# Kernel optimization log

Measured on AMD Instinct MI355X. Metric: run time of the kernel, lower is better.

The kernel has to match this reference:

```python
import jax, jax.numpy as jnp
import numpy as np

B, N, FEAT, MSG, LINK_H, CLS = 8, 128, 1024, 256, 512, 600
PROP = 2  # propagate_layers


def setup_inputs() -> dict:
    key = jax.random.key(0)
    ks = jax.random.split(key, 16)
    g = lambda k, shape, s=0.02: jax.random.normal(k, shape, dtype=jnp.float32) * s
    inp = {
        'edge_features': g(ks[0], (B, N, N, FEAT), 1.0),
        'node_features': g(ks[1], (B, N, FEAT), 1.0),
        'adj_mat': jnp.zeros((B, N, N), jnp.float32),          # shape placeholder only
        'node_labels': jnp.zeros((B, N, CLS), jnp.float32),    # shape placeholder only
        'human_nums': 64,
        'obj_nums': 64,
        # feature resize linears (Linear(FEAT -> MSG))
        'W_er': g(ks[2], (MSG, FEAT)), 'b_er': jnp.zeros((MSG,), jnp.float32),
        'W_nr': g(ks[3], (MSG, FEAT)), 'b_nr': jnp.zeros((MSG,), jnp.float32),
        # link fun (GraphConv): 1x1 Conv2d(MSG->LINK_H), ReLU, 1x1 Conv2d(LINK_H->1)
        'W_l1': g(ks[4], (LINK_H, MSG)), 'b_l1': jnp.zeros((LINK_H,), jnp.float32),
        'W_l2': g(ks[5], (1, LINK_H)), 'b_l2': jnp.zeros((1,), jnp.float32),
        # message fun linear_concat_relu: Linear(node+edge = 2*MSG -> MSG), ReLU
        'W_m': g(ks[6], (MSG, 2 * MSG)), 'b_m': jnp.zeros((MSG,), jnp.float32),
        # GRU(input=MSG, hidden=MSG), single layer single step
        'W_ih': g(ks[7], (3 * MSG, MSG)), 'b_ih': jnp.zeros((3 * MSG,), jnp.float32),
        'W_hh': g(ks[8], (3 * MSG, MSG)), 'b_hh': jnp.zeros((3 * MSG,), jnp.float32),
        # readout fc: Linear(MSG -> CLS)
        'W_r': g(ks[9], (CLS, MSG)), 'b_r': jnp.zeros((CLS,), jnp.float32),
    }
    return inp


def reference(edge_features, node_features, adj_mat, node_labels,
              human_nums, obj_nums,
              W_er, b_er, W_nr, b_nr, W_l1, b_l1, W_l2, b_l2,
              W_m, b_m, W_ih, b_ih, W_hh, b_hh, W_r, b_r):
    # valid_node_num = human_nums + obj_nums == N for every batch element.
    # Resize raw features to message size.
    e = edge_features @ W_er.T + b_er        # [B, v, w, MSG]
    h = node_features @ W_nr.T + b_nr        # [B, w, MSG]  (node states are never rewritten in source)
    # Split concat-linear into two matmuls to avoid materializing [B,N,N,2*MSG].
    W_mh, W_me = W_m[:, :MSG], W_m[:, MSG:]
    msg_h = jnp.einsum('bwd,md->bwm', h, W_mh)                 # node part, shared over target v
    msg_e = jnp.einsum('bvwd,md->bvwm', e, W_me) + b_m          # edge part (original e, constant over rounds)
    edge_state = e
    m = None
    pred_adj = None
    for _ in range(PROP):
        # link fun: per-(v,w) MLP over channels (1x1 convs)
        x = jax.nn.relu(edge_state @ W_l1.T + b_l1)             # [B,v,w,LINK_H]
        pred_adj = (x @ W_l2.T + b_l2)[..., 0]                  # [B,N,N]
        sig = jax.nn.sigmoid(pred_adj)
        # message fun linear_concat_relu, gated by predicted adjacency
        m = jax.nn.relu(msg_h[:, None, :, :] + msg_e)           # [B,v,w,MSG]
        m = sig[..., None] * m
        # hidden_edge_states[round+1][:, :, w, v] = m_v[:, :, w]
        edge_state = jnp.swapaxes(m, 1, 2)
    # node update happens per node each round but hidden node states are never
    # written back in the source, so only the last round's GRU step matters.
    m_sum = m.sum(axis=2)                                       # [B,v,MSG]
    gi = m_sum @ W_ih.T + b_ih
    gh = h @ W_hh.T + b_hh
    ir, iz, inn = jnp.split(gi, 3, axis=-1)
    hr, hz, hn = jnp.split(gh, 3, axis=-1)
    r = jax.nn.sigmoid(ir + hr)
    z = jax.nn.sigmoid(iz + hz)
    n = jnp.tanh(inn + r * hn)
    h_new = (1.0 - z) * n + z * h                               # [B,N,MSG]
    pred_node_labels = h_new @ W_r.T + b_r                      # [B,N,CLS]
    return pred_adj, pred_node_labels
```

## Files before the change

kernel.cpp:

```cpp
#include <hip/hip_runtime.h>
#include <cstdint>
#include <cstddef>

#define NND   128
#define FEATD 1024
#define MSGD  256
#define LHD   512
#define CLSD  600
#define LDST  264

typedef __bf16 bf16_t;
typedef bf16_t bf16x8 __attribute__((ext_vector_type(8)));
typedef float  f32x4  __attribute__((ext_vector_type(4)));
typedef unsigned short u16;
typedef u16 u16x8 __attribute__((ext_vector_type(8)));
typedef u16 u16x4 __attribute__((ext_vector_type(4)));

static __device__ __forceinline__ float bf2f(u16 u) {
  union { unsigned u; float f; } x; x.u = ((unsigned)u) << 16; return x.f;
}
static __device__ __forceinline__ u16 f2bf(float f) {
  union { float f; unsigned u; } x; x.f = f;
  return (u16)((x.u + 0x7fffu + ((x.u >> 16) & 1u)) >> 16);
}
static __device__ __forceinline__ f32x4 mfma16(u16x8 a, u16x8 b, f32x4 c) {
  return __builtin_amdgcn_mfma_f32_16x16x32_bf16(
      __builtin_bit_cast(bf16x8, a), __builtin_bit_cast(bf16x8, b), c, 0, 0, 0);
}
static __device__ __forceinline__ f32x4 zero4() {
  f32x4 v; v[0] = 0.f; v[1] = 0.f; v[2] = 0.f; v[3] = 0.f; return v;
}
static __device__ __forceinline__ float sigm(float x) { return 1.0f / (1.0f + expf(-x)); }

__global__ void k_cvt(const float* __restrict__ src, u16* __restrict__ dst, int n) {
  int i = (blockIdx.x * 256 + threadIdx.x) * 4;
  if (i + 3 < n) {
    float4 f = *(const float4*)(src + i);
    u16x4 o; o[0] = f2bf(f.x); o[1] = f2bf(f.y); o[2] = f2bf(f.z); o[3] = f2bf(f.w);
    *(u16x4*)(dst + i) = o;
  }
}

__global__ __launch_bounds__(256) void k_comb(const float* __restrict__ Wm,
                                              const float* __restrict__ Wer,
                                              const float* __restrict__ b_er,
                                              const float* __restrict__ b_m,
                                              u16* __restrict__ WcombB,
                                              float* __restrict__ bcomb) {
  const int m = blockIdx.x >> 2, ch = blockIdx.x & 3;
  const int d = ch * 256 + threadIdx.x;
  float s = 0.f;
  for (int k = 0; k < 256; ++k)
    s += Wm[(size_t)m * 512 + 256 + k] * Wer[(size_t)k * FEATD + d];
  WcombB[(size_t)m * FEATD + d] = f2bf(s);
  if (ch == 0 && threadIdx.x == 0) {
    float bb2 = b_m[m];
    for (int k = 0; k < 256; ++k) bb2 += Wm[(size_t)m * 512 + 256 + k] * b_er[k];
    bcomb[m] = bb2;
  }
}

__global__ __launch_bounds__(256) void s1_hmsg(const float* __restrict__ node,
                                               const float* __restrict__ Wnr,
                                               const float* __restrict__ bnr,
                                               const float* __restrict__ Wm,
                                               float* __restrict__ h32,
                                               u16* __restrict__ msghB) {
  __shared__ float nrow[FEATD];
  __shared__ float hrow[MSGD];
  const int r = blockIdx.x;
  const int t = threadIdx.x;
  *(float4*)(&nrow[t * 4]) = *(const float4*)(node + (size_t)r * FEATD + t * 4);
  __syncthreads();
  float acc = bnr[t];
  for (int d = 0; d < FEATD; ++d) acc += nrow[d] * Wnr[(size_t)t * FEATD + d];
  h32[(size_t)r * MSGD + t] = acc;
  hrow[t] = acc;
  __syncthreads();
  float mh = 0.f;
  for (int k = 0; k < MSGD; ++k) mh += hrow[k] * Wm[(size_t)t * 2 * MSGD + k];
  msghB[(size_t)r * MSGD + t] = f2bf(mh);
}

__global__ __launch_bounds__(256, 2) void k_main(
    const float* __restrict__ edge, const u16* __restrict__ Wer, const u16* __restrict__ Wm,
    const u16* __restrict__ Wl1, const float* __restrict__ b_er, const float* __restrict__ b_m,
    const float* __restrict__ b_l1, const float* __restrict__ W_l2, const float* __restrict__ b_l2,
    const u16* __restrict__ msgh, u16* __restrict__ M0g, float* __restrict__ pa_out) {
  __shared__ __align__(16) u16 lsE[64][LDST];
  __shared__ __align__(16) u16 lsM[64][LDST];
  __shared__ float lsPA[4][64];
  __shared__ float lsSig[64];

  const int tid = threadIdx.x, lane = tid & 63, wave = tid >> 6;
  const int lh = lane & 15, lq = lane >> 4;
  const int base = blockIdx.x * 64;
  const int bb = base >> 14, vv = (base >> 7) & 127, w0 = base & 127;

  f32x4 acc[4][4];
#pragma unroll
  for (int m = 0; m < 4; ++m)
#pragma unroll
    for (int t = 0; t < 4; ++t) acc[m][t] = zero4();

  const int srow = tid >> 2;
  const int scq  = (tid & 3) * 16;
  const float* esrc = edge + (size_t)(base + srow) * FEATD + scq;
  float4 lda[4], ldb[4];

  auto LOADS_A = [&](int s) {
#pragma unroll
    for (int i = 0; i < 4; ++i) lda[i] = *(const float4*)(esrc + s * 64 + i * 4);
  };
  auto LOADS_B = [&](int s) {
#pragma unroll
    for (int i = 0; i < 4; ++i) ldb[i] = *(const float4*)(esrc + s * 64 + i * 4);
  };
  auto WRITES = [&](const float4* ld, int slot) {
    u16* wp = &lsE[srow][slot * 64 + scq];
    u16x8 o0, o1;
    o0[0] = f2bf(ld[0].x); o0[1] = f2bf(ld[0].y); o0[2] = f2bf(ld[0].z); o0[3] = f2bf(ld[0].w);
    o0[4] = f2bf(ld[1].x); o0[5] = f2bf(ld[1].y); o0[6] = f2bf(ld[1].z); o0[7] = f2bf(ld[1].w);
    o1[0] = f2bf(ld[2].x); o1[1] = f2bf(ld[2].y); o1[2] = f2bf(ld[2].z); o1[3] = f2bf(ld[2].w);
    o1[4] = f2bf(ld[3].x); o1[5] = f2bf(ld[3].y); o1[6] = f2bf(ld[3].z); o1[7] = f2bf(ld[3].w);
    *(u16x8*)wp = o0;
    *(u16x8*)(wp + 8) = o1;
  };
  auto MSTEP = [&](int sk, int slot) {
#pragma unroll
    for (int ks = 0; ks < 2; ++ks) {
      u16x8 afr[4];
#pragma unroll
      for (int m = 0; m < 4; ++m)
        afr[m] = *(const u16x8*)(&lsE[16 * m + lh][slot * 64 + ks * 32 + lq * 8]);
      const int kg = sk * 64 + ks * 32 + lq * 8;
#pragma unroll
      for (int t = 0; t < 4; ++t) {
        int col = wave * 64 + t * 16 + lh;
        u16x8 bfr = *(const u16x8*)(Wer + (size_t)col * FEATD + kg);
#pragma unroll
        for (int m = 0; m < 4; ++m) acc[m][t] = mfma16(afr[m], bfr, acc[m][t]);
      }
    }
  };

  LOADS_A(0);
  LOADS_B(1);
  for (int s2 = 0; s2 < 16; s2 += 2) {
    WRITES(lda, 0);
    if (s2 + 2 < 16) LOADS_A(s2 + 2);
    __syncthreads();
    MSTEP(s2, 0);
    WRITES(ldb, 1);
    if (s2 + 3 < 16) LOADS_B(s2 + 3);
    __syncthreads();
    MSTEP(s2 + 1, 1);
  }
  __syncthreads();
#pragma unroll
  for (int t = 0; t < 4; ++t) {
    int col = wave * 64 + t * 16 + lh;
    float be = b_er[col];
#pragma unroll
    for (int m = 0; m < 4; ++m)
#pragma unroll
      for (int j = 0; j < 4; ++j)
        lsE[16 * m + 4 * lq + j][col] = f2bf(acc[m][t][j] + be);
  }
  __syncthreads();

  float prow[4][4];
#pragma unroll
  for (int m = 0; m < 4; ++m)
#pragma unroll
    for (int j = 0; j < 4; ++j) prow[m][j] = 0.f;
#pragma unroll
  for (int np = 0; np < 2; ++np) {
#pragma unroll
    for (int m = 0; m < 4; ++m)
#pragma unroll
      for (int t = 0; t < 4; ++t) acc[m][t] = zero4();
#pragma unroll
    for (int ks = 0; ks < 8; ++ks) {
      u16x8 afr[4];
#pragma unroll
      for (int m = 0; m < 4; ++m) afr[m] = *(const u16x8*)(&lsE[16 * m + lh][ks * 32 + lq * 8]);
      const int kg = ks * 32 + lq * 8;
#pragma unroll
      for (int t = 0; t < 4; ++t) {
        int col = wave * 128 + np * 64 + t * 16 + lh;
        u16x8 bfr = *(const u16x8*)(Wl1 + (size_t)col * MSGD + kg);
#pragma unroll
        for (int m = 0; m < 4; ++m) acc[m][t] = mfma16(afr[m], bfr, acc[m][t]);
      }
    }
#pragma unroll
    for (int t = 0; t < 4; ++t) {
      int col = wave * 128 + np * 64 + t * 16 + lh;
      float bl = b_l1[col], wl = W_l2[col];
#pragma unroll
      for (int m = 0; m < 4; ++m)
#pragma unroll
        for (int j = 0; j < 4; ++j) prow[m][j] += fmaxf(acc[m][t][j] + bl, 0.f) * wl;
    }
  }
#pragma unroll
  for (int off = 1; off < 16; off <<= 1)
#pragma unroll
    for (int m = 0; m < 4; ++m)
#pragma unroll
      for (int j = 0; j < 4; ++j) prow[m][j] += __shfl_xor(prow[m][j], off, 64);
  if (lh == 0) {
#pragma unroll
    for (int m = 0; m < 4; ++m)
#pragma unroll
      for (int j = 0; j < 4; ++j) lsPA[wave][16 * m + 4 * lq + j] = prow[m][j];
  }
  __syncthreads();
  if (tid < 64) {
    float pa1 = lsPA[0][tid] + lsPA[1][tid] + lsPA[2][tid] + lsPA[3][tid] + b_l2[0];
    lsSig[tid] = sigm(pa1);
  }
#pragma unroll
  for (int i = 0; i < 8; ++i) {
    int idx = tid + i * 256;
    int row = idx >> 5;
    int c8 = (idx & 31) << 3;
    *(u16x8*)(&lsM[row][c8]) =
        *(const u16x8*)(msgh + (size_t)(bb * NND + w0 + row) * MSGD + c8);
  }
  __syncthreads();

#pragma unroll
  for (int m = 0; m < 4; ++m)
#pragma unroll
    for (int t = 0; t < 4; ++t) acc[m][t] = zero4();
#pragma unroll
  for (int ks = 0; ks < 8; ++ks) {
    u16x8 afr[4];
#pragma unroll
    for (int m = 0; m < 4; ++m) afr[m] = *(const u16x8*)(&lsE[16 * m + lh][ks * 32 + lq * 8]);
    const int kg = ks * 32 + lq * 8;
#pragma unroll
    for (int t = 0; t < 4; ++t) {
      int col = wave * 64 + t * 16 + lh;
      u16x8 bfr = *(const u16x8*)(Wm + (size_t)col * 512 + 256 + kg);
#pragma unroll
      for (int m = 0; m < 4; ++m) acc[m][t] = mfma16(afr[m], bfr, acc[m][t]);
    }
  }
#pragma unroll
  for (int t = 0; t < 4; ++t) {
    int col = wave * 64 + t * 16 + lh;
    float bm = b_m[col];
#pragma unroll
    for (int m = 0; m < 4; ++m)
#pragma unroll
      for (int j = 0; j < 4; ++j) {
        int row = 16 * m + 4 * lq + j;
        float mh = bf2f(lsM[row][col]);
        lsM[row][col] = f2bf(fmaxf(acc[m][t][j] + bm + mh, 0.f));
      }
  }
  __syncthreads();
#pragma unroll
  for (int i = 0; i < 8; ++i) {
    int idx = tid + i * 256;
    int row = idx >> 5;
    int c8 = (idx & 31) << 3;
    u16x8 m0v = *(const u16x8*)(&lsM[row][c8]);
    if (M0g) *(u16x8*)(M0g + (size_t)(base + row) * MSGD + c8) = m0v;
    float s = lsSig[row];
    u16x8 sc;
#pragma unroll
    for (int j = 0; j < 8; ++j) sc[j] = f2bf(bf2f(m0v[j]) * s);
    *(u16x8*)(&lsM[row][c8]) = sc;
  }
  __syncthreads();

#pragma unroll
  for (int m = 0; m < 4; ++m)
#pragma unroll
    for (int j = 0; j < 4; ++j) prow[m][j] = 0.f;
#pragma unroll
  for (int np = 0; np < 2; ++np) {
#pragma unroll
    for (int m = 0; m < 4; ++m)
#pragma unroll
      for (int t = 0; t < 4; ++t) acc[m][t] = zero4();
#pragma unroll
    for (int ks = 0; ks < 8; ++ks) {
      u16x8 afr[4];
#pragma unroll
      for (int m = 0; m < 4; ++m) afr[m] = *(const u16x8*)(&lsM[16 * m + lh][ks * 32 + lq * 8]);
      const int kg = ks * 32 + lq * 8;
#pragma unroll
      for (int t = 0; t < 4; ++t) {
        int col = wave * 128 + np * 64 + t * 16 + lh;
        u16x8 bfr = *(const u16x8*)(Wl1 + (size_t)col * MSGD + kg);
#pragma unroll
        for (int m = 0; m < 4; ++m) acc[m][t] = mfma16(afr[m], bfr, acc[m][t]);
      }
    }
#pragma unroll
    for (int t = 0; t < 4; ++t) {
      int col = wave * 128 + np * 64 + t * 16 + lh;
      float bl = b_l1[col], wl = W_l2[col];
#pragma unroll
      for (int m = 0; m < 4; ++m)
#pragma unroll
        for (int j = 0; j < 4; ++j) prow[m][j] += fmaxf(acc[m][t][j] + bl, 0.f) * wl;
    }
  }
#pragma unroll
  for (int off = 1; off < 16; off <<= 1)
#pragma unroll
    for (int m = 0; m < 4; ++m)
#pragma unroll
      for (int j = 0; j < 4; ++j) prow[m][j] += __shfl_xor(prow[m][j], off, 64);
  if (lh == 0) {
#pragma unroll
    for (int m = 0; m < 4; ++m)
#pragma unroll
      for (int j = 0; j < 4; ++j) lsPA[wave][16 * m + 4 * lq + j] = prow[m][j];
  }
  __syncthreads();
  if (tid < 64) {
    float q = lsPA[0][tid] + lsPA[1][tid] + lsPA[2][tid] + lsPA[3][tid] + b_l2[0];
    size_t o = ((size_t)bb * NND + (w0 + tid)) * NND + vv;
    pa_out[o] = q;
  }
}

__global__ __launch_bounds__(256) void k_msum_lite(const u16* __restrict__ M0g,
                                                   const float* __restrict__ qv,
                                                   float* __restrict__ msum) {
  __shared__ float sig[128];
  const int bv = blockIdx.x, tid = threadIdx.x;
  if (tid < 128) sig[tid] = sigm(qv[(size_t)bv * NND + tid]);
  __syncthreads();
  const u16* p = M0g + (size_t)bv * NND * MSGD + tid;
  float a = 0.f;
#pragma unroll 8
  for (int w = 0; w < 128; ++w) a += sig[w] * bf2f(p[(size_t)w * MSGD]);
  msum[(size_t)bv * MSGD + tid] = a;
}

__global__ __launch_bounds__(256, 2) void k_msum2(
    const float* __restrict__ edge, const u16* __restrict__ Wcomb,
    const float* __restrict__ bcomb, const u16* __restrict__ msgh,
    const float* __restrict__ qv, float* __restrict__ msum) {
  __shared__ __align__(16) u16 lsE[64][LDST];
  __shared__ __align__(16) u16 lsM[64][LDST];
  __shared__ float lsSig[64];
  const int tid = threadIdx.x, lane = tid & 63, wave = tid >> 6;
  const int lh = lane & 15, lq = lane >> 4;
  const int bv = blockIdx.x;
  const int bb = bv >> 7;

  float csum[4] = {0.f, 0.f, 0.f, 0.f};

  for (int hh = 0; hh < 2; ++hh) {
    if (tid < 64) lsSig[tid] = sigm(qv[(size_t)bv * NND + hh * 64 + tid]);
#pragma unroll
    for (int i = 0; i < 8; ++i) {
      int idx = tid + i * 256;
      int row = idx >> 5;
      int c8 = (idx & 31) << 3;
      *(u16x8*)(&lsM[row][c8]) =
          *(const u16x8*)(msgh + (size_t)(bb * NND + hh * 64 + row) * MSGD + c8);
    }
    f32x4 acc[4][4];
#pragma unroll
    for (int m = 0; m < 4; ++m)
#pragma unroll
      for (int t = 0; t < 4; ++t) acc[m][t] = zero4();

    for (int kc = 0; kc < 4; ++kc) {
#pragma unroll
      for (int i = 0; i < 16; ++i) {
        int idx = tid + i * 256;
        int row = idx >> 6;
        int c4 = (idx & 63) << 2;
        float4 f = *(const float4*)(edge + (size_t)(bv * NND + hh * 64 + row) * FEATD + kc * 256 + c4);
        u16x4 o; o[0] = f2bf(f.x); o[1] = f2bf(f.y); o[2] = f2bf(f.z); o[3] = f2bf(f.w);
        *(u16x4*)(&lsE[row][c4]) = o;
      }
      __syncthreads();
#pragma unroll
      for (int ks = 0; ks < 8; ++ks) {
        u16x8 afr[4];
#pragma unroll
        for (int m = 0; m < 4; ++m) afr[m] = *(const u16x8*)(&lsE[16 * m + lh][ks * 32 + lq * 8]);
        const int kg = kc * 256 + ks * 32 + lq * 8;
#pragma unroll
        for (int t = 0; t < 4; ++t) {
          int col = wave * 64 + t * 16 + lh;
          u16x8 bfr = *(const u16x8*)(Wcomb + (size_t)col * FEATD + kg);
#pragma unroll
          for (int m = 0; m < 4; ++m) acc[m][t] = mfma16(afr[m], bfr, acc[m][t]);
        }
      }
      __syncthreads();
    }
#pragma unroll
    for (int t = 0; t < 4; ++t) {
      int col = wave * 64 + t * 16 + lh;
      float bc = bcomb[col];
#pragma unroll
      for (int m = 0; m < 4; ++m)
#pragma unroll
        for (int j = 0; j < 4; ++j) {
          int row = 16 * m + 4 * lq + j;
          float m0 = fmaxf(acc[m][t][j] + bc + bf2f(lsM[row][col]), 0.f);
          csum[t] += lsSig[row] * m0;
        }
    }
    __syncthreads();
  }
#pragma unroll
  for (int off = 16; off < 64; off <<= 1)
#pragma unroll
    for (int t = 0; t < 4; ++t) csum[t] += __shfl_xor(csum[t], off, 64);
  if (lq == 0) {
#pragma unroll
    for (int t = 0; t < 4; ++t)
      msum[(size_t)bv * MSGD + wave * 64 + t * 16 + lh] = csum[t];
  }
}

__global__ __launch_bounds__(256) void k_gru(const float* __restrict__ msum,
                                             const float* __restrict__ h32,
                                             const float* __restrict__ Wih, const float* __restrict__ bih,
                                             const float* __restrict__ Whh, const float* __restrict__ bhh,
                                             const float* __restrict__ Wr, const float* __restrict__ br,
                                             float* __restrict__ outlab) {
  __shared__ __align__(16) float sM[8][256];
  __shared__ __align__(16) float sH[8][256];
  __shared__ __align__(16) float sHn[8][256];
  const int tid = threadIdx.x;
  const int r0 = blockIdx.x * 8;
#pragma unroll
  for (int i = 0; i < 2; ++i) {
    int idx = tid + i * 256;
    int row = idx >> 6;
    int c = (idx & 63) << 2;
    *(float4*)(&sM[row][c]) = *(const float4*)(msum + (size_t)(r0 + row) * 256 + c);
    *(float4*)(&sH[row][c]) = *(const float4*)(h32 + (size_t)(r0 + row) * 256 + c);
  }
  __syncthreads();
  float gi[3][8], gh[3][8];
#pragma unroll
  for (int c = 0; c < 3; ++c) {
    float bi_ = bih[tid + 256 * c], bh_ = bhh[tid + 256 * c];
#pragma unroll
    for (int rr = 0; rr < 8; ++rr) { gi[c][rr] = bi_; gh[c][rr] = bh_; }
  }
  for (int k = 0; k < 256; k += 4) {
    float4 wi[3], wh[3];
#pragma unroll
    for (int c = 0; c < 3; ++c) {
      wi[c] = *(const float4*)(Wih + (size_t)(tid + 256 * c) * 256 + k);
      wh[c] = *(const float4*)(Whh + (size_t)(tid + 256 * c) * 256 + k);
    }
#pragma unroll
    for (int rr = 0; rr < 8; ++rr) {
      float4 ms = *(const float4*)(&sM[rr][k]);
      float4 hh = *(const float4*)(&sH[rr][k]);
#pragma unroll
      for (int c = 0; c < 3; ++c) {
        gi[c][rr] += wi[c].x * ms.x + wi[c].y * ms.y + wi[c].z * ms.z + wi[c].w * ms.w;
        gh[c][rr] += wh[c].x * hh.x + wh[c].y * hh.y + wh[c].z * hh.z + wh[c].w * hh.w;
      }
    }
  }
#pragma unroll
  for (int rr = 0; rr < 8; ++rr) {
    float r = sigm(gi[0][rr] + gh[0][rr]);
    float z = sigm(gi[1][rr] + gh[1][rr]);
    float n = tanhf(gi[2][rr] + r * gh[2][rr]);
    sHn[rr][tid] = (1.f - z) * n + z * sH[rr][tid];
  }
  __syncthreads();
  float lab[3][8];
  int cs[3]; bool has[3];
#pragma unroll
  for (int c = 0; c < 3; ++c) {
    cs[c] = tid + 256 * c;
    has[c] = cs[c] < CLSD;
    float b0 = has[c] ? br[cs[c]] : 0.f;
#pragma unroll
    for (int rr = 0; rr < 8; ++rr) lab[c][rr] = b0;
  }
  for (int k = 0; k < 256; k += 4) {
    float4 wr[3];
#pragma unroll
    for (int c = 0; c < 3; ++c) {
      if (has[c]) wr[c] = *(const float4*)(Wr + (size_t)cs[c] * 256 + k);
      else { wr[c].x = 0.f; wr[c].y = 0.f; wr[c].z = 0.f; wr[c].w = 0.f; }
    }
#pragma unroll
    for (int rr = 0; rr < 8; ++rr) {
      float4 hv = *(const float4*)(&sHn[rr][k]);
#pragma unroll
      for (int c = 0; c < 3; ++c)
        lab[c][rr] += wr[c].x * hv.x + wr[c].y * hv.y + wr[c].z * hv.z + wr[c].w * hv.w;
    }
  }
#pragma unroll
  for (int c = 0; c < 3; ++c) {
    if (has[c]) {
#pragma unroll
      for (int rr = 0; rr < 8; ++rr)
        outlab[(size_t)(r0 + rr) * CLSD + cs[c]] = lab[c][rr];
    }
  }
}

extern "C" void kernel_launch(void* const* d_in, const int* in_sizes, int n_in,
                              void* d_out, int out_size, void* d_ws, size_t ws_size,
                              hipStream_t stream) {
  const float* edge = (const float*)d_in[0];
  const float* node = (const float*)d_in[1];
  const float* W_er = (const float*)d_in[6];
  const float* b_er = (const float*)d_in[7];
  const float* W_nr = (const float*)d_in[8];
  const float* b_nr = (const float*)d_in[9];
  const float* W_l1 = (const float*)d_in[10];
  const float* b_l1 = (const float*)d_in[11];
  const float* W_l2 = (const float*)d_in[12];
  const float* b_l2 = (const float*)d_in[13];
  const float* W_m  = (const float*)d_in[14];
  const float* b_m  = (const float*)d_in[15];
  const float* W_ih = (const float*)d_in[16];
  const float* b_ih = (const float*)d_in[17];
  const float* W_hh = (const float*)d_in[18];
  const float* b_hh = (const float*)d_in[19];
  const float* W_r  = (const float*)d_in[20];
  const float* b_r  = (const float*)d_in[21];

  char* ws = (char*)d_ws;
  size_t off = 0;
  auto alloc = [&](size_t bytes) -> void* {
    void* p = ws + off;
    off += (bytes + 511) & ~(size_t)511;
    return p;
  };
  u16* WerB     = (u16*)alloc((size_t)262144 * 2);
  u16* WmB      = (u16*)alloc((size_t)131072 * 2);
  u16* Wl1B     = (u16*)alloc((size_t)131072 * 2);
  u16* WcombB   = (u16*)alloc((size_t)262144 * 2);
  float* bcombF = (float*)alloc((size_t)256 * 4);
  u16* msghB    = (u16*)alloc((size_t)262144 * 2);
  float* h32    = (float*)alloc((size_t)262144 * 4);
  float* msum   = (float*)alloc((size_t)262144 * 4);
  u16* M0g      = (u16*)alloc((size_t)33554432 * 2);
  size_t off_m0 = off;
  const bool fast = (ws_size >= off_m0);
  u16* M0arg = fast ? M0g : (u16*)nullptr;

  float* out_pa  = (float*)d_out;
  float* out_lab = out_pa + 131072;

  k_cvt  <<<256,  256, 0, stream>>>(W_er, WerB, 262144);
  k_cvt  <<<128,  256, 0, stream>>>(W_m,  WmB,  131072);
  k_cvt  <<<128,  256, 0, stream>>>(W_l1, Wl1B, 131072);
  s1_hmsg<<<1024, 256, 0, stream>>>(node, W_nr, b_nr, W_m, h32, msghB);
  if (!fast)
    k_comb<<<1024, 256, 0, stream>>>(W_m, W_er, b_er, b_m, WcombB, bcombF);

  k_main<<<2048, 256, 0, stream>>>(edge, WerB, WmB, Wl1B, b_er, b_m, b_l1, W_l2, b_l2,
                                   msghB, M0arg, out_pa);
  if (fast)
    k_msum_lite<<<1024, 256, 0, stream>>>(M0g, out_pa, msum);
  else
    k_msum2<<<1024, 256, 0, stream>>>(edge, WcombB, bcombF, msghB, out_pa, msum);
  k_gru<<<128, 256, 0, stream>>>(msum, h32, W_ih, b_ih, W_hh, b_hh, W_r, b_r, out_lab);
}
```

Measured before the change: 715.3 us.

## Prefetch weight fragments into registers ahead of MFMA and vectorize msum reduction

In the main fused kernel, the global loads of B-operand weight fragments for the edge-resize GEMM are issued before the barrier, alongside the A-tile loads, so their latency overlaps the sync. The Wl1 and Wm GEMMs now double-buffer the next k-step's fragments in registers while MFMAs run on the current ones. The msum kernel changes from scalar strided bf16 loads to 16-byte vector loads per thread, followed by a shared-memory partial reduction. The extra live registers may cost occupancy under the 2-blocks-per-SM launch bound, or cause spills.

```diff
diff --git a/kernel.cpp b/kernel.cpp
--- a/kernel.cpp
+++ b/kernel.cpp
@@ -82,7 +82,7 @@
   msghB[(size_t)r * MSGD + t] = f2bf(mh);
 }
 
-__global__ __launch_bounds__(256, 2) void k_main(
+__global__ __launch_bounds__(256, 2) void k_main_full(
     const float* __restrict__ edge, const u16* __restrict__ Wer, const u16* __restrict__ Wm,
     const u16* __restrict__ Wl1, const float* __restrict__ b_er, const float* __restrict__ b_m,
     const float* __restrict__ b_l1, const float* __restrict__ W_l2, const float* __restrict__ b_l2,
@@ -107,6 +107,7 @@
   const int scq  = (tid & 3) * 16;
   const float* esrc = edge + (size_t)(base + srow) * FEATD + scq;
   float4 lda[4], ldb[4];
+  u16x8 bst[2][4];
 
   auto LOADS_A = [&](int s) {
 #pragma unroll
@@ -126,21 +127,26 @@
     *(u16x8*)wp = o0;
     *(u16x8*)(wp + 8) = o1;
   };
-  auto MSTEP = [&](int sk, int slot) {
+  auto BLOAD = [&](int sk) {
+#pragma unroll
+    for (int ks = 0; ks < 2; ++ks)
+#pragma unroll
+      for (int t = 0; t < 4; ++t) {
+        int col = wave * 64 + t * 16 + lh;
+        bst[ks][t] = *(const u16x8*)(Wer + (size_t)col * FEATD + sk * 64 + ks * 32 + lq * 8);
+      }
+  };
+  auto MCOMP = [&](int slot) {
 #pragma unroll
     for (int ks = 0; ks < 2; ++ks) {
       u16x8 afr[4];
 #pragma unroll
       for (int m = 0; m < 4; ++m)
         afr[m] = *(const u16x8*)(&lsE[16 * m + lh][slot * 64 + ks * 32 + lq * 8]);
-      const int kg = sk * 64 + ks * 32 + lq * 8;
-#pragma unroll
-      for (int t = 0; t < 4; ++t) {
-        int col = wave * 64 + t * 16 + lh;
-        u16x8 bfr = *(const u16x8*)(Wer + (size_t)col * FEATD + kg);
-#pragma unroll
-        for (int m = 0; m < 4; ++m) acc[m][t] = mfma16(afr[m], bfr, acc[m][t]);
-      }
+#pragma unroll
+      for (int t = 0; t < 4; ++t)
+#pragma unroll
+        for (int m = 0; m < 4; ++m) acc[m][t] = mfma16(afr[m], bst[ks][t], acc[m][t]);
     }
   };
 
@@ -149,12 +155,14 @@
   for (int s2 = 0; s2 < 16; s2 += 2) {
     WRITES(lda, 0);
     if (s2 + 2 < 16) LOADS_A(s2 + 2);
+    BLOAD(s2);
     __syncthreads();
-    MSTEP(s2, 0);
+    MCOMP(0);
     WRITES(ldb, 1);
     if (s2 + 3 < 16) LOADS_B(s2 + 3);
+    BLOAD(s2 + 1);
     __syncthreads();
-    MSTEP(s2 + 1, 1);
+    MCOMP(1);
   }
   __syncthreads();
 #pragma unroll
@@ -180,18 +188,29 @@
     for (int m = 0; m < 4; ++m)
 #pragma unroll
       for (int t = 0; t < 4; ++t) acc[m][t] = zero4();
+    u16x8 bcur[4];
+#pragma unroll
+    for (int t = 0; t < 4; ++t)
+      bcur[t] = *(const u16x8*)(Wl1 + (size_t)(wave * 128 + np * 64 + t * 16 + lh) * MSGD + lq * 8);
 #pragma unroll
     for (int ks = 0; ks < 8; ++ks) {
+      u16x8 bnxt[4];
+      if (ks < 7) {
+#pragma unroll
+        for (int t = 0; t < 4; ++t)
+          bnxt[t] = *(const u16x8*)(Wl1 + (size_t)(wave * 128 + np * 64 + t * 16 + lh) * MSGD +
+                                    (ks + 1) * 32 + lq * 8);
+      }
       u16x8 afr[4];
 #pragma unroll
       for (int m = 0; m < 4; ++m) afr[m] = *(const u16x8*)(&lsE[16 * m + lh][ks * 32 + lq * 8]);
-      const int kg = ks * 32 + lq * 8;
-#pragma unroll
-      for (int t = 0; t < 4; ++t) {
-        int col = wave * 128 + np * 64 + t * 16 + lh;
-        u16x8 bfr = *(const u16x8*)(Wl1 + (size_t)col * MSGD + kg);
-#pragma unroll
-        for (int m = 0; m < 4; ++m) acc[m][t] = mfma16(afr[m], bfr, acc[m][t]);
+#pragma unroll
+      for (int t = 0; t < 4; ++t)
+#pragma unroll
+        for (int m = 0; m < 4; ++m) acc[m][t] = mfma16(afr[m], bcur[t], acc[m][t]);
+      if (ks < 7) {
+#pragma unroll
+        for (int t = 0; t < 4; ++t) bcur[t] = bnxt[t];
       }
     }
 #pragma unroll
@@ -235,18 +254,31 @@
   for (int m = 0; m < 4; ++m)
 #pragma unroll
     for (int t = 0; t < 4; ++t) acc[m][t] = zero4();
-#pragma unroll
-  for (int ks = 0; ks < 8; ++ks) {
-    u16x8 afr[4];
-#pragma unroll
-    for (int m = 0; m < 4; ++m) afr[m] = *(const u16x8*)(&lsE[16 * m + lh][ks * 32 + lq * 8]);
-    const int kg = ks * 32 + lq * 8;
-#pragma unroll
-    for (int t = 0; t < 4; ++t) {
-      int col = wave * 64 + t * 16 + lh;
-      u16x8 bfr = *(const u16x8*)(Wm + (size_t)col * 512 + 256 + kg);
-#pragma unroll
-      for (int m = 0; m < 4; ++m) acc[m][t] = mfma16(afr[m], bfr, acc[m][t]);
+  {
+    u16x8 bcur[4];
+#pragma unroll
+    for (int t = 0; t < 4; ++t)
+      bcur[t] = *(const u16x8*)(Wm + (size_t)(wave * 64 + t * 16 + lh) * 512 + 256 + lq * 8);
+#pragma unroll
+    for (int ks = 0; ks < 8; ++ks) {
+      u16x8 bnxt[4];
+      if (ks < 7) {
+#pragma unroll
+        for (int t = 0; t < 4; ++t)
+          bnxt[t] = *(const u16x8*)(Wm + (size_t)(wave * 64 + t * 16 + lh) * 512 + 256 +
+                                    (ks + 1) * 32 + lq * 8);
+      }
+      u16x8 afr[4];
+#pragma unroll
+      for (int m = 0; m < 4; ++m) afr[m] = *(const u16x8*)(&lsE[16 * m + lh][ks * 32 + lq * 8]);
+#pragma unroll
+      for (int t = 0; t < 4; ++t)
+#pragma unroll
+        for (int m = 0; m < 4; ++m) acc[m][t] = mfma16(afr[m], bcur[t], acc[m][t]);
+      if (ks < 7) {
+#pragma unroll
+        for (int t = 0; t < 4; ++t) bcur[t] = bnxt[t];
+      }
     }
   }
 #pragma unroll
@@ -288,18 +320,29 @@
     for (int m = 0; m < 4; ++m)
 #pragma unroll
       for (int t = 0; t < 4; ++t) acc[m][t] = zero4();
+    u16x8 bcur[4];
+#pragma unroll
+    for (int t = 0; t < 4; ++t)
+      bcur[t] = *(const u16x8*)(Wl1 + (size_t)(wave * 128 + np * 64 + t * 16 + lh) * MSGD + lq * 8);
 #pragma unroll
     for (int ks = 0; ks < 8; ++ks) {
+      u16x8 bnxt[4];
+      if (ks < 7) {
+#pragma unroll
+        for (int t = 0; t < 4; ++t)
+          bnxt[t] = *(const u16x8*)(Wl1 + (size_t)(wave * 128 + np * 64 + t * 16 + lh) * MSGD +
+                                    (ks + 1) * 32 + lq * 8);
+      }
       u16x8 afr[4];
 #pragma unroll
       for (int m = 0; m < 4; ++m) afr[m] = *(const u16x8*)(&lsM[16 * m + lh][ks * 32 + lq * 8]);
-      const int kg = ks * 32 + lq * 8;
-#pragma unroll
-      for (int t = 0; t < 4; ++t) {
-        int col = wave * 128 + np * 64 + t * 16 + lh;
-        u16x8 bfr = *(const u16x8*)(Wl1 + (size_t)col * MSGD + kg);
-#pragma unroll
-        for (int m = 0; m < 4; ++m) acc[m][t] = mfma16(afr[m], bfr, acc[m][t]);
+#pragma unroll
+      for (int t = 0; t < 4; ++t)
+#pragma unroll
+        for (int m = 0; m < 4; ++m) acc[m][t] = mfma16(afr[m], bcur[t], acc[m][t]);
+      if (ks < 7) {
+#pragma unroll
+        for (int t = 0; t < 4; ++t) bcur[t] = bnxt[t];
       }
     }
 #pragma unroll
@@ -336,14 +379,28 @@
                                                    const float* __restrict__ qv,
                                                    float* __restrict__ msum) {
   __shared__ float sig[128];
+  __shared__ __align__(16) float part[8][256];
   const int bv = blockIdx.x, tid = threadIdx.x;
   if (tid < 128) sig[tid] = sigm(qv[(size_t)bv * NND + tid]);
   __syncthreads();
-  const u16* p = M0g + (size_t)bv * NND * MSGD + tid;
-  float a = 0.f;
-#pragma unroll 8
-  for (int w = 0; w < 128; ++w) a += sig[w] * bf2f(p[(size_t)w * MSGD]);
-  msum[(size_t)bv * MSGD + tid] = a;
+  const int cg = (tid & 31) * 8, rg = tid >> 5;
+  float a[8];
+#pragma unroll
+  for (int j = 0; j < 8; ++j) a[j] = 0.f;
+  for (int i = 0; i < 16; ++i) {
+    int row = rg + i * 8;
+    u16x8 v = *(const u16x8*)(M0g + ((size_t)bv * NND + row) * MSGD + cg);
+    float s = sig[row];
+#pragma unroll
+    for (int j = 0; j < 8; ++j) a[j] += s * bf2f(v[j]);
+  }
+#pragma unroll
+  for (int j = 0; j < 8; ++j) part[rg][cg + j] = a[j];
+  __syncthreads();
+  float r = 0.f;
+#pragma unroll
+  for (int g = 0; g < 8; ++g) r += part[g][tid];
+  msum[(size_t)bv * MSGD + tid] = r;
 }
 
 __global__ __launch_bounds__(256, 2) void k_msum2(
@@ -569,8 +626,8 @@
   if (!fast)
     k_comb<<<1024, 256, 0, stream>>>(W_m, W_er, b_er, b_m, WcombB, bcombF);
 
-  k_main<<<2048, 256, 0, stream>>>(edge, WerB, WmB, Wl1B, b_er, b_m, b_l1, W_l2, b_l2,
-                                   msghB, M0arg, out_pa);
+  k_main_full<<<2048, 256, 0, stream>>>(edge, WerB, WmB, Wl1B, b_er, b_m, b_l1, W_l2, b_l2,
+                                        msghB, M0arg, out_pa);
   if (fast)
     k_msum_lite<<<1024, 256, 0, stream>>>(M0g, out_pa, msum);
   else
```

Result: faster. 693.9 us (-3.0%).
